# Performance work log

Measured on AMD Instinct MI355X. Metric: run time of the kernel, lower is better.

Reference implementation:

```python
import jax, jax.numpy as jnp
import numpy as np

N = 100000
E = 3200000
F_IN = 256
HID = 128


def _dconv_k1(x_cat, w, b):
    # torch_geometric_temporal DConv with K=1:
    # H = X @ W[0,0] + X @ W[1,0] + b   (no graph propagation for K=1)
    return x_cat @ (w[0, 0] + w[1, 0]) + b


def _dcrnn_cell(x, h, wz, bz, wr, br, wh, bh):
    xh = jnp.concatenate([x, h], axis=1)
    z = jax.nn.sigmoid(_dconv_k1(xh, wz, bz))
    r = jax.nn.sigmoid(_dconv_k1(xh, wr, br))
    xrh = jnp.concatenate([x, r * h], axis=1)
    h_tilde = jnp.tanh(_dconv_k1(xrh, wh, bh))
    return z * h + (1.0 - z) * h_tilde


def setup_inputs() -> dict:
    key = jax.random.key(0)
    ks = jax.random.split(key, 16)

    def gw(k, shape):
        fan_in = shape[-2]
        return jax.random.normal(k, shape, dtype=jnp.float32) / np.sqrt(fan_in)

    inp = {
        "x": jax.random.normal(ks[0], (N, F_IN), dtype=jnp.float32),
        "edge_index": jax.random.randint(ks[1], (2, E), 0, N, dtype=jnp.int64 if jax.config.jax_enable_x64 else jnp.int32),
        "edge_weight": jax.random.uniform(ks[2], (E,), dtype=jnp.float32),
        "w_z1": gw(ks[3], (2, 1, F_IN + HID, HID)), "b_z1": jnp.zeros((HID,), jnp.float32),
        "w_r1": gw(ks[4], (2, 1, F_IN + HID, HID)), "b_r1": jnp.zeros((HID,), jnp.float32),
        "w_h1": gw(ks[5], (2, 1, F_IN + HID, HID)), "b_h1": jnp.zeros((HID,), jnp.float32),
        "w_z2": gw(ks[6], (2, 1, HID + HID // 2, HID // 2)), "b_z2": jnp.zeros((HID // 2,), jnp.float32),
        "w_r2": gw(ks[7], (2, 1, HID + HID // 2, HID // 2)), "b_r2": jnp.zeros((HID // 2,), jnp.float32),
        "w_h2": gw(ks[8], (2, 1, HID + HID // 2, HID // 2)), "b_h2": jnp.zeros((HID // 2,), jnp.float32),
        "w_lin1": gw(ks[9], (HID // 2, 16)), "b_lin1": jnp.zeros((16,), jnp.float32),
        "w_lin2": gw(ks[10], (16, 1)), "b_lin2": jnp.zeros((1,), jnp.float32),
    }
    return inp


def reference(x, edge_index, edge_weight,
              w_z1, b_z1, w_r1, b_r1, w_h1, b_h1,
              w_z2, b_z2, w_r2, b_r2, w_h2, b_h2,
              w_lin1, b_lin1, w_lin2, b_lin2):
    # edge_index / edge_weight are unused in the K=1 DConv math (faithful to tgt source).
    h0 = jnp.zeros((x.shape[0], w_z1.shape[-1]), x.dtype)
    h = _dcrnn_cell(x, h0, w_z1, b_z1, w_r1, b_r1, w_h1, b_h1)
    h = jax.nn.relu(h)
    h0b = jnp.zeros((x.shape[0], w_z2.shape[-1]), x.dtype)
    h = _dcrnn_cell(h, h0b, w_z2, b_z2, w_r2, b_r2, w_h2, b_h2)
    h = jax.nn.relu(h)
    # Dropout(0.2) is identity at inference
    h = jax.nn.relu(h @ w_lin1 + b_lin1)
    return h @ w_lin2 + b_lin2
```

## Files before the change

### kernel.cpp

```cpp
#include <hip/hip_runtime.h>

typedef _Float16 f16;
typedef _Float16 f16x4 __attribute__((ext_vector_type(4)));
typedef _Float16 f16x8 __attribute__((ext_vector_type(8)));
typedef float    f32x4 __attribute__((ext_vector_type(4)));

#define N_ROWS 100000
#define RT 1563
#define LSH1 136
#define LSH2 72

#define W1T_OFF 0
#define W1T_BYTES (256 * 256 * 2)
#define W2T_OFF W1T_BYTES

__device__ __forceinline__ void glds16(const void* g, void* l) {
    __builtin_amdgcn_global_load_lds((const __attribute__((address_space(1))) void*)g,
                                     (__attribute__((address_space(3))) void*)l, 16, 0, 0);
}

__global__ void prep_w(const float* __restrict__ wz1, const float* __restrict__ wh1,
                       const float* __restrict__ wz2, const float* __restrict__ wh2,
                       f16* __restrict__ W1T, f16* __restrict__ W2T) {
    const int b = blockIdx.x;
    if (b < 256) {
        int idx = b * 256 + threadIdx.x;
        int k = idx >> 8, c = idx & 255;
        const float* w = (c < 128) ? wz1 : wh1;
        int cc = c & 127;
        W1T[c * 256 + k] = (f16)(w[k * 128 + cc] + w[384 * 128 + k * 128 + cc]);
    } else {
        int idx = (b - 256) * 256 + threadIdx.x;
        int k = idx >> 7, c = idx & 127;
        const float* w = (c < 64) ? wz2 : wh2;
        int cc = c & 63;
        W2T[c * 128 + k] = (f16)(w[k * 64 + cc] + w[192 * 64 + k * 64 + cc]);
    }
}

__global__ __launch_bounds__(256, 2) void fused(
    const float* __restrict__ x,
    const f16* __restrict__ W1T, const f16* __restrict__ W2T,
    const float* __restrict__ bz1, const float* __restrict__ bh1,
    const float* __restrict__ bz2, const float* __restrict__ bh2,
    const float* __restrict__ wl1, const float* __restrict__ bl1,
    const float* __restrict__ wl2, const float* __restrict__ bl2,
    float* __restrict__ out)
{
    __shared__ __align__(16) float Xs[64 * 256];
    f16* h1s = (f16*)Xs;
    f16* h2s = (f16*)((char*)Xs + 17408);

    const int tid = threadIdx.x, lane = tid & 63, wave = tid >> 6;
    const int ln = lane & 15, quad = lane >> 4;
    const int r0 = blockIdx.x * 64;

#pragma unroll
    for (int t = 0; t < 16; ++t) {
        const int r = wave * 16 + t;
        int gr = r0 + r; if (gr >= N_ROWS) gr = N_ROWS - 1;
        glds16(x + (size_t)gr * 256 + (((lane ^ r) & 63) << 2), &Xs[r * 256]);
    }

    const f16* wbase[4];
#pragma unroll
    for (int mi = 0; mi < 4; ++mi) {
        const int M = (mi < 2) ? (2 * wave + mi) : (8 + 2 * wave + mi - 2);
        wbase[mi] = W1T + (size_t)(M * 16 + ln) * 256 + quad * 8;
    }
    f16x8 wc[4], wn[4];
#pragma unroll
    for (int mi = 0; mi < 4; ++mi) wc[mi] = *(const f16x8*)(wbase[mi]);

    __syncthreads();

    f32x4 acc[4][4];
#pragma unroll
    for (int a = 0; a < 4; ++a)
#pragma unroll
        for (int b = 0; b < 4; ++b) acc[a][b] = (f32x4){0.f, 0.f, 0.f, 0.f};

#pragma unroll
    for (int kc = 0; kc < 8; ++kc) {
#pragma unroll
        for (int mi = 0; mi < 4; ++mi)
            wn[mi] = *(const f16x8*)(wbase[mi] + (kc + 1) * 32);
        f16x8 bf[4];
#pragma unroll
        for (int nt = 0; nt < 4; ++nt) {
            const int row = 16 * nt + ln;
            const int c0 = kc * 8 + 2 * quad;
            float4 a = *(const float4*)&Xs[row * 256 + ((c0 ^ row) << 2)];
            float4 b = *(const float4*)&Xs[row * 256 + (((c0 + 1) ^ row) << 2)];
            bf[nt] = (f16x8){(f16)a.x,(f16)a.y,(f16)a.z,(f16)a.w,
                             (f16)b.x,(f16)b.y,(f16)b.z,(f16)b.w};
        }
#pragma unroll
        for (int mi = 0; mi < 4; ++mi)
#pragma unroll
            for (int nt = 0; nt < 4; ++nt)
                acc[mi][nt] = __builtin_amdgcn_mfma_f32_16x16x32_f16(wc[mi], bf[nt], acc[mi][nt], 0, 0, 0);
#pragma unroll
        for (int mi = 0; mi < 4; ++mi) wc[mi] = wn[mi];
    }
    __syncthreads();

    f16x8 w2f[2][4];
#pragma unroll
    for (int kc = 0; kc < 4; ++kc) {
        w2f[0][kc] = *(const f16x8*)(W2T + (size_t)(16 * wave + ln) * 128 + kc * 32 + quad * 8);
        w2f[1][kc] = *(const f16x8*)(W2T + (size_t)(64 + 16 * wave + ln) * 128 + kc * 32 + quad * 8);
    }

#pragma unroll
    for (int mi = 0; mi < 2; ++mi) {
        const int jg0 = 32 * wave + 16 * mi + (quad << 2);
        const float4 zb = *(const float4*)(bz1 + jg0);
        const float4 hb = *(const float4*)(bh1 + jg0);
#pragma unroll
        for (int nt = 0; nt < 4; ++nt) {
            const int row = 16 * nt + ln;
            f16x4 pk;
#pragma unroll
            for (int i = 0; i < 4; ++i) {
                float zp = acc[mi][nt][i]     + (&zb.x)[i];
                float hp = acc[mi + 2][nt][i] + (&hb.x)[i];
                float ex = __expf(2.0f * hp);
                float th = 1.0f - 2.0f / (ex + 1.0f);
                float sg = 1.0f / (1.0f + __expf(zp));
                pk[i] = (f16)fmaxf(th * sg, 0.0f);
            }
            *(f16x4*)&h1s[row * LSH1 + jg0] = pk;
        }
    }
    __syncthreads();

    f32x4 acc2[2][4];
#pragma unroll
    for (int a = 0; a < 2; ++a)
#pragma unroll
        for (int b = 0; b < 4; ++b) acc2[a][b] = (f32x4){0.f, 0.f, 0.f, 0.f};
#pragma unroll
    for (int kc = 0; kc < 4; ++kc) {
        f16x8 bf[4];
#pragma unroll
        for (int nt = 0; nt < 4; ++nt)
            bf[nt] = *(const f16x8*)&h1s[(16 * nt + ln) * LSH1 + kc * 32 + quad * 8];
#pragma unroll
        for (int m = 0; m < 2; ++m)
#pragma unroll
            for (int nt = 0; nt < 4; ++nt)
                acc2[m][nt] = __builtin_amdgcn_mfma_f32_16x16x32_f16(w2f[m][kc], bf[nt], acc2[m][nt], 0, 0, 0);
    }
    __syncthreads();

    {
        const int jg0 = 16 * wave + (quad << 2);
        const float4 zb = *(const float4*)(bz2 + jg0);
        const float4 hb = *(const float4*)(bh2 + jg0);
#pragma unroll
        for (int nt = 0; nt < 4; ++nt) {
            const int row = 16 * nt + ln;
            f16x4 pk;
#pragma unroll
            for (int i = 0; i < 4; ++i) {
                float zp = acc2[0][nt][i] + (&zb.x)[i];
                float hp = acc2[1][nt][i] + (&hb.x)[i];
                float ex = __expf(2.0f * hp);
                float th = 1.0f - 2.0f / (ex + 1.0f);
                float sg = 1.0f / (1.0f + __expf(zp));
                pk[i] = (f16)fmaxf(th * sg, 0.0f);
            }
            *(f16x4*)&h2s[row * LSH2 + jg0] = pk;
        }
    }
    __syncthreads();

    const float blv = bl1[ln], wlv = wl2[ln], bl2v = bl2[0];
    f16x8 bfr[2];
#pragma unroll
    for (int kc = 0; kc < 2; ++kc)
#pragma unroll
        for (int j = 0; j < 8; ++j)
            bfr[kc][j] = (f16)wl1[(32 * kc + 8 * quad + j) * 16 + ln];

    f32x4 acc3 = (f32x4){0.f, 0.f, 0.f, 0.f};
#pragma unroll
    for (int kc = 0; kc < 2; ++kc) {
        f16x8 af = *(const f16x8*)&h2s[(16 * wave + ln) * LSH2 + kc * 32 + quad * 8];
        acc3 = __builtin_amdgcn_mfma_f32_16x16x32_f16(af, bfr[kc], acc3, 0, 0, 0);
    }
#pragma unroll
    for (int i = 0; i < 4; ++i) {
        float v = fmaxf(acc3[i] + blv, 0.0f) * wlv;
        v += __shfl_xor(v, 1);
        v += __shfl_xor(v, 2);
        v += __shfl_xor(v, 4);
        v += __shfl_xor(v, 8);
        if (ln == 0) {
            const int row = r0 + 16 * wave + (quad << 2) + i;
            if (row < N_ROWS) out[row] = v + bl2v;
        }
    }
}

extern "C" void kernel_launch(void* const* d_in, const int* in_sizes, int n_in,
                              void* d_out, int out_size, void* d_ws, size_t ws_size,
                              hipStream_t stream) {
    const float* x   = (const float*)d_in[0];
    const float* wz1 = (const float*)d_in[3];
    const float* bz1 = (const float*)d_in[4];
    const float* wh1 = (const float*)d_in[7];
    const float* bh1 = (const float*)d_in[8];
    const float* wz2 = (const float*)d_in[9];
    const float* bz2 = (const float*)d_in[10];
    const float* wh2 = (const float*)d_in[13];
    const float* bh2 = (const float*)d_in[14];
    const float* wl1 = (const float*)d_in[15];
    const float* bl1 = (const float*)d_in[16];
    const float* wl2 = (const float*)d_in[17];
    const float* bl2 = (const float*)d_in[18];

    char* ws = (char*)d_ws;
    f16* W1T = (f16*)(ws + W1T_OFF);
    f16* W2T = (f16*)(ws + W2T_OFF);
    float* out = (float*)d_out;

    prep_w<<<320, 256, 0, stream>>>(wz1, wh1, wz2, wh2, W1T, W2T);
    fused<<<RT, 256, 0, stream>>>(x, W1T, W2T, bz1, bh1, bz2, bh2,
                                  wl1, bl1, wl2, bl2, out);
}
```

Baseline: 244.4 us.

## Stage x tile as fp16 in padded LDS via registers, raise occupancy

Replaces the direct global-to-LDS fp32 load of the x tile with register loads that convert to fp16 and store into a padded fp16 LDS buffer. This halves LDS footprint (about 33KB vs 64KB), allowing launch bounds to request 4 blocks per CU, and removes the per-iteration fp32-to-fp16 conversion and XOR swizzle in the GEMM loop. It also avoids an out-of-bounds weight prefetch on the last k-chunk and drops a barrier between the second GEMM and its epilogue. The risk is losing the async LDS load path, added register pressure from holding 16 float4 per thread, and a possible race since h2s is written right after h1s reads without a barrier (h2s lives in a separate region, so likely safe).

```diff
diff --git a/kernel.cpp b/kernel.cpp
--- a/kernel.cpp
+++ b/kernel.cpp
@@ -7,17 +7,13 @@
 
 #define N_ROWS 100000
 #define RT 1563
+#define LSX 264
 #define LSH1 136
 #define LSH2 72
 
 #define W1T_OFF 0
 #define W1T_BYTES (256 * 256 * 2)
 #define W2T_OFF W1T_BYTES
-
-__device__ __forceinline__ void glds16(const void* g, void* l) {
-    __builtin_amdgcn_global_load_lds((const __attribute__((address_space(1))) void*)g,
-                                     (__attribute__((address_space(3))) void*)l, 16, 0, 0);
-}
 
 __global__ void prep_w(const float* __restrict__ wz1, const float* __restrict__ wh1,
                        const float* __restrict__ wz2, const float* __restrict__ wh2,
@@ -38,7 +34,7 @@
     }
 }
 
-__global__ __launch_bounds__(256, 2) void fused(
+__global__ __launch_bounds__(256, 4) void fused(
     const float* __restrict__ x,
     const f16* __restrict__ W1T, const f16* __restrict__ W2T,
     const float* __restrict__ bz1, const float* __restrict__ bh1,
@@ -47,20 +43,26 @@
     const float* __restrict__ wl2, const float* __restrict__ bl2,
     float* __restrict__ out)
 {
-    __shared__ __align__(16) float Xs[64 * 256];
-    f16* h1s = (f16*)Xs;
-    f16* h2s = (f16*)((char*)Xs + 17408);
+    __shared__ __align__(16) f16 Xs[64 * LSX];
+    f16* h1s = Xs;
+    f16* h2s = Xs + 8704;
 
     const int tid = threadIdx.x, lane = tid & 63, wave = tid >> 6;
     const int ln = lane & 15, quad = lane >> 4;
     const int r0 = blockIdx.x * 64;
 
-#pragma unroll
-    for (int t = 0; t < 16; ++t) {
-        const int r = wave * 16 + t;
-        int gr = r0 + r; if (gr >= N_ROWS) gr = N_ROWS - 1;
-        glds16(x + (size_t)gr * 256 + (((lane ^ r) & 63) << 2), &Xs[r * 256]);
-    }
+    const int sr = tid >> 2;
+    const int sc = (tid & 3) << 3;
+    int gsr = r0 + sr; if (gsr >= N_ROWS) gsr = N_ROWS - 1;
+    const float* xp = x + (size_t)gsr * 256 + sc;
+
+    float4 va[8], vb[8];
+#pragma unroll
+    for (int g = 0; g < 8; ++g) {
+        va[g] = *(const float4*)(xp + g * 32);
+        vb[g] = *(const float4*)(xp + g * 32 + 4);
+    }
+    __builtin_amdgcn_sched_barrier(0);
 
     const f16* wbase[4];
 #pragma unroll
@@ -68,10 +70,15 @@
         const int M = (mi < 2) ? (2 * wave + mi) : (8 + 2 * wave + mi - 2);
         wbase[mi] = W1T + (size_t)(M * 16 + ln) * 256 + quad * 8;
     }
-    f16x8 wc[4], wn[4];
+    f16x8 wc[4];
 #pragma unroll
     for (int mi = 0; mi < 4; ++mi) wc[mi] = *(const f16x8*)(wbase[mi]);
 
+#pragma unroll
+    for (int g = 0; g < 8; ++g)
+        *(f16x8*)&Xs[sr * LSX + sc + g * 32] =
+            (f16x8){(f16)va[g].x,(f16)va[g].y,(f16)va[g].z,(f16)va[g].w,
+                    (f16)vb[g].x,(f16)vb[g].y,(f16)vb[g].z,(f16)vb[g].w};
     __syncthreads();
 
     f32x4 acc[4][4];
@@ -80,28 +87,29 @@
 #pragma unroll
         for (int b = 0; b < 4; ++b) acc[a][b] = (f32x4){0.f, 0.f, 0.f, 0.f};
 
+    const f16* xrd = &Xs[ln * LSX + quad * 8];
+
 #pragma unroll
     for (int kc = 0; kc < 8; ++kc) {
-#pragma unroll
-        for (int mi = 0; mi < 4; ++mi)
-            wn[mi] = *(const f16x8*)(wbase[mi] + (kc + 1) * 32);
+        f16x8 wn[4];
+        if (kc < 7) {
+#pragma unroll
+            for (int mi = 0; mi < 4; ++mi)
+                wn[mi] = *(const f16x8*)(wbase[mi] + (kc + 1) * 32);
+        }
         f16x8 bf[4];
 #pragma unroll
-        for (int nt = 0; nt < 4; ++nt) {
-            const int row = 16 * nt + ln;
-            const int c0 = kc * 8 + 2 * quad;
-            float4 a = *(const float4*)&Xs[row * 256 + ((c0 ^ row) << 2)];
-            float4 b = *(const float4*)&Xs[row * 256 + (((c0 + 1) ^ row) << 2)];
-            bf[nt] = (f16x8){(f16)a.x,(f16)a.y,(f16)a.z,(f16)a.w,
-                             (f16)b.x,(f16)b.y,(f16)b.z,(f16)b.w};
-        }
+        for (int nt = 0; nt < 4; ++nt)
+            bf[nt] = *(const f16x8*)(xrd + nt * 16 * LSX + kc * 32);
 #pragma unroll
         for (int mi = 0; mi < 4; ++mi)
 #pragma unroll
             for (int nt = 0; nt < 4; ++nt)
                 acc[mi][nt] = __builtin_amdgcn_mfma_f32_16x16x32_f16(wc[mi], bf[nt], acc[mi][nt], 0, 0, 0);
-#pragma unroll
-        for (int mi = 0; mi < 4; ++mi) wc[mi] = wn[mi];
+        if (kc < 7) {
+#pragma unroll
+            for (int mi = 0; mi < 4; ++mi) wc[mi] = wn[mi];
+        }
     }
     __syncthreads();
 
@@ -152,7 +160,6 @@
             for (int nt = 0; nt < 4; ++nt)
                 acc2[m][nt] = __builtin_amdgcn_mfma_f32_16x16x32_f16(w2f[m][kc], bf[nt], acc2[m][nt], 0, 0, 0);
     }
-    __syncthreads();
 
     {
         const int jg0 = 16 * wave + (quad << 2);
```

Measured after the change: 242.1 us. No clear change (-0.9%).
